# Performance work log

Measured on AMD Instinct MI355X. Metric: run time of the kernel, lower is better.

The kernel has to match this reference:

```python
import jax, jax.numpy as jnp
import numpy as np

EMBED, HID, INSIDE, OUTSIDE, EPS = 128, 64, 4, 8, 1e-5
N_NODES, N_EDGES, BATCH, SEQLEN = 16384, 262144, 64, 21


def _layernorm(x, g, b):
    m = x.mean(-1, keepdims=True)
    v = ((x - m) ** 2).mean(-1, keepdims=True)
    return (x - m) * jax.lax.rsqrt(v + EPS) * g + b


def _lstm_dir(x, Wih, Whh, bih, bhh, reverse):
    # x: [B, L, D] -> h: [B, L, HID]; PyTorch gate order i,f,g,o
    pre = jnp.einsum('bld,gd->blg', x, Wih) + bih + bhh  # [B,L,4H]
    pre = jnp.swapaxes(pre, 0, 1)  # [L,B,4H]
    h0 = jnp.zeros((x.shape[0], HID), x.dtype)

    def step(carry, xt):
        h, c = carry
        gates = xt + h @ Whh.T
        i, f, g, o = jnp.split(gates, 4, axis=-1)
        c = jax.nn.sigmoid(f) * c + jax.nn.sigmoid(i) * jnp.tanh(g)
        h = jax.nn.sigmoid(o) * jnp.tanh(c)
        return (h, c), h

    _, hs = jax.lax.scan(step, (h0, h0), pre, reverse=reverse)
    return jnp.swapaxes(hs, 0, 1)


def setup_inputs():
    key = jax.random.key(0)
    ks = jax.random.split(key, 40)
    f = jnp.float32
    N, E, B, L, D = N_NODES, N_EDGES, BATCH, SEQLEN, EMBED

    def w(k, shape, fan_in):
        return jax.random.normal(k, shape, f) * (1.0 / np.sqrt(fan_in))

    inp = {
        'x': jax.random.normal(ks[0], (N, 2561), f),
        'edge_index': jax.random.randint(ks[1], (2, E), 0, N, jnp.int32),
        'edge_attr': jax.random.normal(ks[2], (E, 3), f),
        # sorted node->graph assignment; every graph id 0..B-1 present
        'batch': ((jnp.arange(N, dtype=jnp.int32) * B) // N).astype(jnp.int32),
        'hotslice': jax.random.normal(ks[3], (B, L, 28), f),
        # randn_like noise tensors from the torch forward, made explicit inputs
        'noise_seqy': jax.random.normal(ks[4], (B, L, D), f),
        'noise_seqz': jax.random.normal(ks[5], (B, L, D), f),
        'noise_sty': jax.random.normal(ks[6], (N, D), f),
        'noise_stz': jax.random.normal(ks[7], (N, D), f),
        # AttnNN params
        'W_esm': w(ks[8], (D, 2560), 2560), 'b_esm': jnp.zeros((D,), f),
        'W_node': w(ks[9], (D, D + 1), D + 1), 'b_node': jnp.zeros((D,), f),
        'W_seq': w(ks[10], (D, 28), 28), 'b_seq': jnp.zeros((D,), f),
        # SeqStructBlock params
        'ln_seq_g': jnp.ones((D,), f), 'ln_seq_b': jnp.zeros((D,), f),
        'ln_st_g': jnp.ones((D,), f), 'ln_st_b': jnp.zeros((D,), f),
        'W_in': w(ks[11], (D, 2 * D + 3), 2 * D + 3), 'b_in': jnp.zeros((D,), f),
        'W_out': w(ks[12], (D, 2 * D + 3), 2 * D + 3), 'b_out': jnp.zeros((D,), f),
        'Wih_f': w(ks[13], (4 * HID, D), HID), 'Whh_f': w(ks[14], (4 * HID, HID), HID),
        'bih_f': jnp.zeros((4 * HID,), f), 'bhh_f': jnp.zeros((4 * HID,), f),
        'Wih_b': w(ks[15], (4 * HID, D), HID), 'Whh_b': w(ks[16], (4 * HID, HID), HID),
        'bih_b': jnp.zeros((4 * HID,), f), 'bhh_b': jnp.zeros((4 * HID,), f),
        # BatchNorm1d (eval mode: running stats)
        'bn_g': jnp.ones((D,), f), 'bn_b': jnp.zeros((D,), f),
        'bn_rm': jnp.zeros((D,), f), 'bn_rv': jnp.ones((D,), f),
    }
    return inp


def reference(x, edge_index, edge_attr, batch, hotslice,
              noise_seqy, noise_seqz, noise_sty, noise_stz,
              W_esm, b_esm, W_node, b_node, W_seq, b_seq,
              ln_seq_g, ln_seq_b, ln_st_g, ln_st_b,
              W_in, b_in, W_out, b_out,
              Wih_f, Whh_f, bih_f, bhh_f, Wih_b, Whh_b, bih_b, bhh_b,
              bn_g, bn_b, bn_rm, bn_rv):
    N = x.shape[0]
    B = hotslice.shape[0]
    src, dst = edge_index[0, 0::2], edge_index[1, 0::2]
    ea_in, ea_out = edge_attr[1::2], edge_attr[0::2]

    def ss(seq, struct):
        # bidirectional LSTM + residual + LayerNorm (dropout = identity, eval)
        hf = _lstm_dir(seq, Wih_f, Whh_f, bih_f, bhh_f, False)
        hb = _lstm_dir(seq, Wih_b, Whh_b, bih_b, bhh_b, True)
        seq = _layernorm(seq + jnp.concatenate([hf, hb], -1), ln_seq_g, ln_seq_b)
        sn = struct
        fs, fd = sn[src], sn[dst]  # [E/2, 128] gathers
        gin = jax.nn.sigmoid(jnp.concatenate([fs, fd, ea_in], -1) @ W_in.T + b_in)
        struct = struct + jax.ops.segment_sum(gin * fd, src, num_segments=N)
        gout = jax.nn.sigmoid(jnp.concatenate([fs, fd, ea_out], -1) @ W_out.T + b_out)
        struct = struct + jax.ops.segment_sum(gout * fs, dst, num_segments=N)
        return seq, _layernorm(struct, ln_st_g, ln_st_b)

    seq0 = hotslice @ W_seq.T + b_seq                       # [B,L,128]
    esm = x[:, 1:] @ W_esm.T + b_esm                        # [N,128]
    struct0 = jnp.concatenate([esm, x[:, :1]], -1) @ W_node.T + b_node  # [N,128]

    def outer(carry):
        sy, sz, ty, tz = carry

        def inner(c, _):
            szc, tzc = c
            return ss(seq0 + sy + szc, struct0 + ty + tzc), None

        (sz, tz), _ = jax.lax.scan(inner, (sz, tz), None, length=INSIDE)
        sy, ty = ss(sy + sz, ty + tz)
        return (sy, sz, ty, tz)

    carry = (noise_seqy, noise_seqz, noise_sty, noise_stz)
    carry, _ = jax.lax.scan(lambda c, _: (outer(c), None), carry, None,
                            length=OUTSIDE - 1)
    sy, sz, ty, tz = outer(carry)

    # middleSelect picks the first node of each consecutive batch run;
    # batch is sorted with every graph id present -> run starts via searchsorted
    starts = jnp.searchsorted(batch, jnp.arange(B, dtype=batch.dtype))
    feat = sy[:, 10, :] + ty[starts]                        # [B,128]
    # BatchNorm1d, eval mode (running stats)
    return (feat - bn_rm) * jax.lax.rsqrt(bn_rv + EPS) * bn_g + bn_b
```

## Files before the change

### kernel.cpp

```cpp
#include <hip/hip_runtime.h>
#include <hip/hip_fp16.h>
#include <math.h>

#define D 128
#define G4 256
#define LSEQ 21
#define EPSF 1e-5f

typedef unsigned short u16;
typedef __attribute__((ext_vector_type(8))) short bf16x8;
typedef __attribute__((ext_vector_type(4))) float f32x4;
typedef __attribute__((ext_vector_type(2))) unsigned u32x2;
typedef __attribute__((ext_vector_type(4))) unsigned u32x4;

#define MFMA16(a,b,c) __builtin_amdgcn_mfma_f32_16x16x32_bf16(a,b,c,0,0,0)

__device__ __forceinline__ float sigf(float x){ return 1.0f/(1.0f+__expf(-x)); }
__device__ __forceinline__ u16 f2bf(float x){
  unsigned u = __float_as_uint(x);
  return (u16)((u + 0x7FFFu + ((u>>16)&1u)) >> 16);
}
__device__ __forceinline__ float bf2f(u16 h){ return __uint_as_float(((unsigned)h)<<16); }
__device__ __forceinline__ unsigned pack_h2(float a, float b){
  __half2 h = __floats2half2_rn(a, b);
  return *(unsigned*)&h;
}
__device__ __forceinline__ float2 unpack_h2(unsigned u){
  __half2 h = *(__half2*)&u;
  return __half22float2(h);
}
__device__ __forceinline__ u16 f2h(float v){ __half h = __float2half(v); return *(u16*)&h; }

__device__ __forceinline__ void edge_acc(u32x4 a, uint2 g, bool valid,
                                         float2 po2, float2 w0, float2 w1, float2 w2,
                                         float& ax, float& ay){
  float e0=__uint_as_float(a.y), e1=__uint_as_float(a.z), e2=__uint_as_float(a.w);
  float2 ps0 = unpack_h2(g.x);
  float2 ps1 = unpack_h2(g.y);
  float gx = po2.x + ps0.x + e0*w0.x + e1*w1.x + e2*w2.x;
  float gy = po2.y + ps1.x + e0*w0.y + e1*w1.y + e2*w2.y;
  float mm = valid ? 1.f : 0.f;
  ax = fmaf(ps0.y*mm, sigf(gx), ax);
  ay = fmaf(ps1.y*mm, sigf(gy), ay);
}

__global__ void k_misc(int* __restrict__ starts, const int* __restrict__ batch, int N, int Bb,
                       float* __restrict__ WEin, float* __restrict__ WEout,
                       const float* __restrict__ W_in, const float* __restrict__ W_out,
                       float* __restrict__ bsum_f, float* __restrict__ bsum_b,
                       const float* __restrict__ bih_f, const float* __restrict__ bhh_f,
                       const float* __restrict__ bih_b, const float* __restrict__ bhh_b){
  int tid = threadIdx.x;
  if (tid < Bb){
    int lo = 0, hi = N;
    while (lo < hi){ int m = (lo+hi)>>1; if (batch[m] < tid) lo = m+1; else hi = m; }
    starts[tid] = lo;
  }
  for (int i = tid; i < 384; i += 256){
    int t = i >> 7, j = i & 127;
    WEin [i] = W_in [(size_t)j*259 + 256 + t];
    WEout[i] = W_out[(size_t)j*259 + 256 + t];
  }
  if (tid < 256){
    bsum_f[tid] = bih_f[tid] + bhh_f[tid];
    bsum_b[tid] = bih_b[tid] + bhh_b[tid];
  }
}

__global__ void k_packB(u16* __restrict__ PB4h, u16* __restrict__ PB4l,
                        u16* __restrict__ PBnh, u16* __restrict__ PBnl,
                        u16* __restrict__ PBEh, u16* __restrict__ PBEl,
                        const float* __restrict__ W_in, const float* __restrict__ W_out,
                        const float* __restrict__ W_node, const float* __restrict__ W_esm){
  int idx = blockIdx.x*256 + threadIdx.x;
  if (idx < 65536){
    int j = idx&7, l=(idx>>3)&63, q=idx>>9;
    int ks = q&3, nt = q>>2;
    int c = nt*16 + (l&15);
    int k = ks*32 + ((l>>4)<<3) + j;
    float v;
    if (c < 128)      v = W_in [(size_t)c*259 + k];
    else if (c < 256) v = W_in [(size_t)(c-128)*259 + 128 + k];
    else if (c < 384) v = W_out[(size_t)(c-256)*259 + k];
    else              v = W_out[(size_t)(c-384)*259 + 128 + k];
    u16 h = f2bf(v);
    PB4h[idx] = h; PB4l[idx] = f2bf(v - bf2f(h));
  } else if (idx < 65536 + 16384){
    int p = idx - 65536;
    int j = p&7, l=(p>>3)&63, q=p>>9;
    int ks = q&3, nt = q>>2;
    int c = nt*16 + (l&15);
    int k = ks*32 + ((l>>4)<<3) + j;
    float v = W_node[(size_t)c*129 + k];
    u16 h = f2bf(v);
    PBnh[p] = h; PBnl[p] = f2bf(v - bf2f(h));
  } else if (idx < 65536 + 16384 + 327680){
    int p = idx - 81920;
    int j = p&7, l=(p>>3)&63, q=p>>9;
    int ks = q%80, nt = q/80;
    int c = nt*16 + (l&15);
    int k = ks*32 + ((l>>4)<<3) + j;
    float v = W_esm[(size_t)c*2560 + k];
    u16 h = f2bf(v);
    PBEh[p] = h; PBEl[p] = f2bf(v - bf2f(h));
  }
}

__global__ void k_seq0(float* __restrict__ seq0, const float* __restrict__ hot,
                       const float* __restrict__ W_seq, const float* __restrict__ b_seq){
  int row = blockIdx.x, j = threadIdx.x;
  const float* h = hot + (size_t)row*28;
  const float* w = W_seq + (size_t)j*28;
  float acc = b_seq[j];
  #pragma unroll
  for (int k = 0; k < 28; k++) acc += h[k]*w[k];
  seq0[(size_t)row*D + j] = acc;
}

__global__ __launch_bounds__(256) void k_esm2(float* __restrict__ struct0, const float* __restrict__ x,
    const u16* __restrict__ PBEh, const u16* __restrict__ PBEl,
    const u16* __restrict__ PBnh, const u16* __restrict__ PBnl,
    const float* __restrict__ b_esm, const float* __restrict__ W_node,
    const float* __restrict__ b_node){
  __shared__ union {
    struct { u16 xh[16*72], xl[16*72]; } p1;
    struct { u16 Ah[16*136], Al[16*136]; } p2;
  } uu;
  __shared__ float esmF[16*132];
  int tid = threadIdx.x;
  int r0 = blockIdx.x*16;
  int w = tid>>6, l = tid&63;
  f32x4 acc[2];
  acc[0] = (f32x4){0.f,0.f,0.f,0.f};
  acc[1] = (f32x4){0.f,0.f,0.f,0.f};

  float xv[4];
  int rr = tid >> 5, k2i = tid & 31;
  #pragma unroll
  for (int q = 0; q < 2; q++){
    const float* src = x + (size_t)(r0+rr+8*q)*2561 + 1 + k2i*2;
    xv[2*q]   = src[0];
    xv[2*q+1] = src[1];
  }
  for (int kc = 0; kc < 2560; kc += 64){
    __syncthreads();
    unsigned* xh32 = (unsigned*)uu.p1.xh;
    unsigned* xl32 = (unsigned*)uu.p1.xl;
    #pragma unroll
    for (int q = 0; q < 2; q++){
      float v0 = xv[2*q], v1 = xv[2*q+1];
      u16 h0 = f2bf(v0), h1 = f2bf(v1);
      u16 l0 = f2bf(v0 - bf2f(h0)), l1 = f2bf(v1 - bf2f(h1));
      int r = rr + 8*q;
      xh32[r*36 + k2i] = (unsigned)h0 | ((unsigned)h1 << 16);
      xl32[r*36 + k2i] = (unsigned)l0 | ((unsigned)l1 << 16);
    }
    __syncthreads();
    if (kc + 64 < 2560){
      #pragma unroll
      for (int q = 0; q < 2; q++){
        const float* src = x + (size_t)(r0+rr+8*q)*2561 + 1 + kc + 64 + k2i*2;
        xv[2*q]   = src[0];
        xv[2*q+1] = src[1];
      }
    }
    #pragma unroll
    for (int ks = 0; ks < 2; ks++){
      bf16x8 ah, al;
      {
        int row = l&15;
        int k = ks*32 + ((l>>4)<<3);
        ah = *(const bf16x8*)&uu.p1.xh[row*72 + k];
        al = *(const bf16x8*)&uu.p1.xl[row*72 + k];
      }
      int ksg = (kc>>5) + ks;
      #pragma unroll
      for (int ctl = 0; ctl < 2; ctl++){
        int nt = w*2 + ctl;
        bf16x8 bh = *(const bf16x8*)&PBEh[((size_t)(nt*80 + ksg)*64 + l)*8];
        bf16x8 bl = *(const bf16x8*)&PBEl[((size_t)(nt*80 + ksg)*64 + l)*8];
        acc[ctl] = MFMA16(ah, bh, acc[ctl]);
        acc[ctl] = MFMA16(al, bh, acc[ctl]);
        acc[ctl] = MFMA16(ah, bl, acc[ctl]);
      }
    }
  }
  __syncthreads();
  int cq = l & 15, rqb = (l>>4)*4;
  #pragma unroll
  for (int ctl = 0; ctl < 2; ctl++){
    int coln = (w*2+ctl)*16 + cq;
    float be = b_esm[coln];
    #pragma unroll
    for (int r = 0; r < 4; r++)
      esmF[(rqb+r)*132 + coln] = acc[ctl][r] + be;
  }
  __syncthreads();
  {
    unsigned* Ah32 = (unsigned*)uu.p2.Ah;
    unsigned* Al32 = (unsigned*)uu.p2.Al;
    int rr2 = tid >> 6, k2 = tid & 63;
    #pragma unroll
    for (int q = 0; q < 4; q++){
      int r = rr2 + 4*q;
      float v0 = esmF[r*132 + k2*2];
      float v1 = esmF[r*132 + k2*2 + 1];
      u16 h0 = f2bf(v0), h1 = f2bf(v1);
      u16 l0 = f2bf(v0 - bf2f(h0)), l1 = f2bf(v1 - bf2f(h1));
      Ah32[r*68 + k2] = (unsigned)h0 | ((unsigned)h1 << 16);
      Al32[r*68 + k2] = (unsigned)l0 | ((unsigned)l1 << 16);
    }
  }
  __syncthreads();
  f32x4 acc2[2];
  acc2[0] = (f32x4){0.f,0.f,0.f,0.f};
  acc2[1] = (f32x4){0.f,0.f,0.f,0.f};
  #pragma unroll
  for (int ks = 0; ks < 4; ks++){
    bf16x8 ah, al;
    {
      int row = l&15;
      int k = ks*32 + ((l>>4)<<3);
      ah = *(const bf16x8*)&uu.p2.Ah[row*136 + k];
      al = *(const bf16x8*)&uu.p2.Al[row*136 + k];
    }
    #pragma unroll
    for (int ctl = 0; ctl < 2; ctl++){
      int nt = w*2 + ctl;
      bf16x8 bh = *(const bf16x8*)&PBnh[((size_t)(nt*4 + ks)*64 + l)*8];
      bf16x8 bl = *(const bf16x8*)&PBnl[((size_t)(nt*4 + ks)*64 + l)*8];
      acc2[ctl] = MFMA16(ah, bh, acc2[ctl]);
      acc2[ctl] = MFMA16(al, bh, acc2[ctl]);
      acc2[ctl] = MFMA16(ah, bl, acc2[ctl]);
    }
  }
  #pragma unroll
  for (int ctl = 0; ctl < 2; ctl++){
    int col = (w*2+ctl)*16 + cq;
    float wl = W_node[(size_t)col*129 + 128];
    float bn = b_node[col];
    #pragma unroll
    for (int r = 0; r < 4; r++){
      int row = r0 + rqb + r;
      float x0 = x[(size_t)row*2561];
      struct0[(size_t)row*D + col] = acc2[ctl][r] + x0*wl + bn;
    }
  }
}

__global__ void k_zero2(int* a, int* b, int n){
  int i = blockIdx.x*blockDim.x + threadIdx.x;
  if (i < n){ a[i] = 0; b[i] = 0; }
}
__global__ void k_count(int* cnt_s, int* cnt_d, const int* __restrict__ ei, int E2){
  int e = blockIdx.x*blockDim.x + threadIdx.x;
  if (e < E2){
    atomicAdd(&cnt_s[ei[2*e]], 1);
    atomicAdd(&cnt_d[ei[2*E2 + 2*e]], 1);
  }
}
__global__ __launch_bounds__(1024) void k_scanp1(const int* __restrict__ cnt_s,
                                                 const int* __restrict__ cnt_d,
                                                 int* __restrict__ part, int n, int nch){
  int arr = blockIdx.x / nch, chunk = blockIdx.x % nch;
  const int* cnt = arr ? cnt_d : cnt_s;
  int i = chunk*1024 + threadIdx.x;
  int v = (i < n) ? cnt[i] : 0;
  __shared__ int ws[16];
  #pragma unroll
  for (int o = 32; o; o >>= 1) v += __shfl_down(v, o);
  if ((threadIdx.x & 63) == 0) ws[threadIdx.x >> 6] = v;
  __syncthreads();
  if (threadIdx.x == 0){
    int t = 0;
    #pragma unroll
    for (int q = 0; q < 16; q++) t += ws[q];
    part[blockIdx.x] = t;
  }
}
__global__ void k_scanp2(int* part, int nch){
  int tid = threadIdx.x;
  if (tid < 2){
    int base = 0;
    for (int i = 0; i < nch; i++){
      int v = part[tid*nch + i];
      part[tid*nch + i] = base;
      base += v;
    }
  }
}
__global__ __launch_bounds__(1024) void k_scanp3(const int* __restrict__ cnt_s,
                                                 const int* __restrict__ cnt_d,
                                                 const int* __restrict__ part,
                                                 int* __restrict__ offs_s, int* __restrict__ offs_d,
                                                 int n, int nch){
  int arr = blockIdx.x / nch, chunk = blockIdx.x % nch;
  const int* cnt = arr ? cnt_d : cnt_s;
  int* offs = arr ? offs_d : offs_s;
  __shared__ int sh[1024];
  int tid = threadIdx.x;
  int i = chunk*1024 + tid;
  int v = (i < n) ? cnt[i] : 0;
  sh[tid] = v;
  __syncthreads();
  for (int off = 1; off < 1024; off <<= 1){
    int t = (tid >= off) ? sh[tid-off] : 0;
    __syncthreads();
    sh[tid] += t;
    __syncthreads();
  }
  int base = part[blockIdx.x];
  if (i < n) offs[i] = base + sh[tid] - v;
  if (i == n-1) offs[n] = base + sh[tid];
}
__global__ void k_copy2(int* cur_s, const int* offs_s, int* cur_d, const int* offs_d, int n){
  int i = blockIdx.x*blockDim.x + threadIdx.x;
  if (i < n){ cur_s[i] = offs_s[i]; cur_d[i] = offs_d[i]; }
}
__global__ void k_fill(const int* __restrict__ ei, const float* __restrict__ eattr, int E2,
                       int* cur_s, int4* __restrict__ adj_s,
                       int* cur_d, int4* __restrict__ adj_d){
  int e = blockIdx.x*blockDim.x + threadIdx.x;
  if (e >= E2) return;
  int s = ei[2*e];
  int d = ei[2*E2 + 2*e];
  const float* ein  = eattr + (size_t)(2*e+1)*3;
  const float* eout = eattr + (size_t)(2*e)*3;
  int ps = atomicAdd(&cur_s[s], 1);
  adj_s[ps] = make_int4(d, __float_as_int(ein[0]),  __float_as_int(ein[1]),  __float_as_int(ein[2]));
  int pd = atomicAdd(&cur_d[d], 1);
  adj_d[pd] = make_int4(s, __float_as_int(eout[0]), __float_as_int(eout[1]), __float_as_int(eout[2]));
}
__global__ void k_pad(int4* __restrict__ adj_s, int4* __restrict__ adj_d, int E2){
  int t = threadIdx.x;
  if (t < 8){
    adj_s[E2+t] = make_int4(0,0,0,0);
    adj_d[E2+t] = make_int4(0,0,0,0);
  }
}

__global__ __launch_bounds__(256) void k_seqA(
  const float* __restrict__ s0s, const float* __restrict__ sy, const float* __restrict__ sz,
  float* __restrict__ seq_in, float* __restrict__ pre_f, float* __restrict__ pre_b,
  const float* __restrict__ Wih_f, const float* __restrict__ Wih_b,
  const float* __restrict__ bsum_f, const float* __restrict__ bsum_b)
{
  __shared__ float sh[LSEQ*128];
  int tid = threadIdx.x;
  int b = blockIdx.x;
  for (int idx = tid; idx < LSEQ*128; idx += 256){
    size_t off = (size_t)b*LSEQ*128 + idx;
    float v = sy[off] + sz[off];
    if (s0s) v += s0s[off];
    sh[idx] = v;
    seq_in[off] = v;
  }
  __syncthreads();
  int g = tid;
  float accf[LSEQ], accb[LSEQ];
  float bf = bsum_f[g], bb = bsum_b[g];
  #pragma unroll
  for (int l = 0; l < LSEQ; l++){ accf[l] = bf; accb[l] = bb; }
  const float* wfp = Wih_f + (size_t)g*128;
  const float* wbp = Wih_b + (size_t)g*128;
  for (int kc = 0; kc < 128; kc += 16){
    float4 wf[4], wb[4];
    #pragma unroll
    for (int q = 0; q < 4; q++){
      wf[q] = *(const float4*)(wfp + kc + 4*q);
      wb[q] = *(const float4*)(wbp + kc + 4*q);
    }
    #pragma unroll
    for (int l = 0; l < LSEQ; l++){
      #pragma unroll
      for (int q = 0; q < 4; q++){
        float4 s4 = *(const float4*)&sh[l*128 + kc + 4*q];
        accf[l] += s4.x*wf[q].x + s4.y*wf[q].y + s4.z*wf[q].z + s4.w*wf[q].w;
        accb[l] += s4.x*wb[q].x + s4.y*wb[q].y + s4.z*wb[q].z + s4.w*wb[q].w;
      }
    }
  }
  for (int l = 0; l < LSEQ; l++){
    pre_f[((size_t)b*LSEQ + l)*G4 + g] = accf[l];
    pre_b[((size_t)b*LSEQ + l)*G4 + g] = accb[l];
  }
}

__global__ __launch_bounds__(256) void k_A(
  const float* __restrict__ s0t, const float* __restrict__ ty, const float* __restrict__ tz,
  const u16* __restrict__ PB4h, const u16* __restrict__ PB4l,
  unsigned* __restrict__ G_in, unsigned* __restrict__ G_out,
  unsigned* __restrict__ PownPk,
  const float* __restrict__ b_in, const float* __restrict__ b_out, int N)
{
  __shared__ struct { u16 Ah[32*136], Al[32*136]; float Sf[32*132]; } m;
  int tid = threadIdx.x;
  int r0 = blockIdx.x*32;
  const float4* ty4 = (const float4*)(ty + (size_t)r0*D);
  const float4* tz4 = (const float4*)(tz + (size_t)r0*D);
  const float4* s04 = s0t ? (const float4*)(s0t + (size_t)r0*D) : nullptr;
  #pragma unroll
  for (int q = 0; q < 4; q++){
    int i = tid + 256*q;
    int r = i >> 5, k4 = i & 31;
    float4 v = ty4[i];
    float4 z = tz4[i];
    v.x += z.x; v.y += z.y; v.z += z.z; v.w += z.w;
    if (s04){ float4 s = s04[i]; v.x += s.x; v.y += s.y; v.z += s.z; v.w += s.w; }
    u16 h0 = f2bf(v.x), h1 = f2bf(v.y), h2 = f2bf(v.z), h3 = f2bf(v.w);
    *(ushort4*)&m.Ah[r*136 + k4*4] = make_ushort4(h0,h1,h2,h3);
    *(ushort4*)&m.Al[r*136 + k4*4] = make_ushort4(
        f2bf(v.x - bf2f(h0)), f2bf(v.y - bf2f(h1)),
        f2bf(v.z - bf2f(h2)), f2bf(v.w - bf2f(h3)));
    *(float4*)&m.Sf[r*132 + k4*4] = v;
  }
  __syncthreads();
  int w = tid >> 6, l = tid & 63;
  f32x4 acc[2][8];
  #pragma unroll
  for (int a=0;a<2;a++)
    #pragma unroll
    for (int b=0;b<8;b++) acc[a][b] = (f32x4){0.f,0.f,0.f,0.f};
  #pragma unroll
  for (int ks = 0; ks < 4; ks++){
    bf16x8 ah[2], al[2];
    #pragma unroll
    for (int rt = 0; rt < 2; rt++){
      int row = rt*16 + (l&15);
      int k = ks*32 + ((l>>4)<<3);
      ah[rt] = *(const bf16x8*)&m.Ah[row*136 + k];
      al[rt] = *(const bf16x8*)&m.Al[row*136 + k];
    }
    #pragma unroll
    for (int ct = 0; ct < 8; ct++){
      int nt = w*8 + ct;
      bf16x8 bh = *(const bf16x8*)&PB4h[((size_t)(nt*4 + ks)*64 + l)*8];
      bf16x8 bl = *(const bf16x8*)&PB4l[((size_t)(nt*4 + ks)*64 + l)*8];
      #pragma unroll
      for (int rt = 0; rt < 2; rt++){
        acc[rt][ct] = MFMA16(ah[rt], bh, acc[rt][ct]);
        acc[rt][ct] = MFMA16(al[rt], bh, acc[rt][ct]);
        acc[rt][ct] = MFMA16(ah[rt], bl, acc[rt][ct]);
      }
    }
  }
  __syncthreads();
  unsigned* stg = (unsigned*)m.Ah;
  u16* stg16 = (u16*)m.Ah;
  int cq = l & 15, rqb = (l>>4)*4;
  if (w == 1){
    #pragma unroll
    for (int ct = 0; ct < 8; ct++){
      int coln = ct*16 + cq;
      #pragma unroll
      for (int rt = 0; rt < 2; rt++){
        #pragma unroll
        for (int r = 0; r < 4; r++){
          int lr = rt*16 + rqb + r;
          stg[lr*128 + coln] = pack_h2(acc[rt][ct][r], m.Sf[lr*132 + coln]);
        }
      }
    }
  }
  __syncthreads();
  {
    uint4* dst = (uint4*)(G_in + (size_t)r0*D);
    const uint4* src = (const uint4*)stg;
    #pragma unroll
    for (int q = 0; q < 4; q++) dst[tid + 256*q] = src[tid + 256*q];
  }
  __syncthreads();
  if (w == 2){
    #pragma unroll
    for (int ct = 0; ct < 8; ct++){
      int coln = ct*16 + cq;
      #pragma unroll
      for (int rt = 0; rt < 2; rt++){
        #pragma unroll
        for (int r = 0; r < 4; r++){
          int lr = rt*16 + rqb + r;
          stg[lr*128 + coln] = pack_h2(acc[rt][ct][r], m.Sf[lr*132 + coln]);
        }
      }
    }
  }
  __syncthreads();
  {
    uint4* dst = (uint4*)(G_out + (size_t)r0*D);
    const uint4* src = (const uint4*)stg;
    #pragma unroll
    for (int q = 0; q < 4; q++) dst[tid + 256*q] = src[tid + 256*q];
  }
  __syncthreads();
  if (w == 0 || w == 3){
    const float* bb = (w == 0) ? b_in : b_out;
    int half = (w == 0) ? 0 : 1;
    #pragma unroll
    for (int ct = 0; ct < 8; ct++){
      int coln = ct*16 + cq;
      float bc = bb[coln];
      #pragma unroll
      for (int rt = 0; rt < 2; rt++){
        #pragma unroll
        for (int r = 0; r < 4; r++){
          int lr = rt*16 + rqb + r;
          stg16[(lr*128 + coln)*2 + half] = f2h(acc[rt][ct][r] + bc);
        }
      }
    }
  }
  __syncthreads();
  {
    uint4* dst = (uint4*)(PownPk + (size_t)r0*D);
    const uint4* src = (const uint4*)stg;
    #pragma unroll
    for (int q = 0; q < 4; q++) dst[tid + 256*q] = src[tid + 256*q];
  }
}

__global__ __launch_bounds__(512) void k_B(
  const unsigned* __restrict__ G_in, const unsigned* __restrict__ G_out,
  const unsigned* __restrict__ PownPk,
  float* __restrict__ to,
  const int* __restrict__ offs_s, const int4* __restrict__ adj_s,
  const int* __restrict__ offs_d, const int4* __restrict__ adj_d,
  const float* __restrict__ WEin, const float* __restrict__ WEout,
  const float* __restrict__ ln_st_g, const float* __restrict__ ln_st_b,
  float* pre_f, float* pre_b,
  const float* __restrict__ Whh_f, const float* __restrict__ Whh_b,
  float* seq_in, float* __restrict__ so,
  const float* __restrict__ otherS, const float* __restrict__ s0s_n,
  const float* __restrict__ Wih_f, const float* __restrict__ Wih_b,
  const float* __restrict__ bsum_f, const float* __restrict__ bsum_b,
  const float* __restrict__ ln_seq_g, const float* __restrict__ ln_seq_b,
  int doNext, int N, int Bb)
{
  __shared__ union {
    struct {
      float h_hist[2][LSEQ][64];
      float hcur[2][64];
      float gsh[2][G4];
      float soL[LSEQ*128];
      float shG[LSEQ*128];
    } sq;
  } u;
  if ((int)blockIdx.x >= Bb){
    int wv = threadIdx.x >> 6, lane = threadIdx.x & 63;
    int n0 = ((blockIdx.x - Bb)*8 + wv)*4;
    const float2* WEi2 = (const float2*)WEin;
    const float2* WEo2 = (const float2*)WEout;
    float2 wi0 = WEi2[lane], wi1 = WEi2[64+lane], wi2 = WEi2[128+lane];
    float2 wo0 = WEo2[lane], wo1 = WEo2[64+lane], wo2 = WEo2[128+lane];
    float2 g2v = ((const float2*)ln_st_g)[lane], be2 = ((const float2*)ln_st_b)[lane];
    const uint2* Gi = (const uint2*)G_in;
    const uint2* Go = (const uint2*)G_out;
    #pragma unroll 1
    for (int n = n0; n < n0+4; ++n){
      u32x2 pw = *((const u32x2*)PownPk + (size_t)n*64 + lane);
      float2 pp0 = unpack_h2(pw.x), pp1 = unpack_h2(pw.y);
      float2 poI = make_float2(pp0.x, pp1.x);
      float2 poO = make_float2(pp0.y, pp1.y);
      uint2 gown = Gi[(size_t)n*64 + lane];
      float ax = 0.f, ay = 0.f;
      int j0 = __builtin_amdgcn_readfirstlane(offs_s[n]);
      int j1 = __builtin_amdgcn_readfirstlane(offs_s[n+1]);
      for (int jb = j0; jb < j1; jb += 4){
        int rem = j1 - jb;
        const u32x4* ap = (const u32x4*)adj_s + jb;
        u32x4 a0 = ap[0], a1 = ap[1], a2 = ap[2], a3 = ap[3];
        uint2 g0 = Gi[(size_t)a0.x*64 + lane];
        uint2 g1 = Gi[(size_t)a1.x*64 + lane];
        uint2 g2 = Gi[(size_t)a2.x*64 + lane];
        uint2 g3 = Gi[(size_t)a3.x*64 + lane];
        edge_acc(a0, g0, true,  poI, wi0, wi1, wi2, ax, ay);
        edge_acc(a1, g1, rem>1, poI, wi0, wi1, wi2, ax, ay);
        edge_acc(a2, g2, rem>2, poI, wi0, wi1, wi2, ax, ay);
        edge_acc(a3, g3, rem>3, poI, wi0, wi1, wi2, ax, ay);
      }
      j0 = __builtin_amdgcn_readfirstlane(offs_d[n]);
      j1 = __builtin_amdgcn_readfirstlane(offs_d[n+1]);
      for (int jb = j0; jb < j1; jb += 4){
        int rem = j1 - jb;
        const u32x4* ap = (const u32x4*)adj_d + jb;
        u32x4 a0 = ap[0], a1 = ap[1], a2 = ap[2], a3 = ap[3];
        uint2 g0 = Go[(size_t)a0.x*64 + lane];
        uint2 g1 = Go[(size_t)a1.x*64 + lane];
        uint2 g2 = Go[(size_t)a2.x*64 + lane];
        uint2 g3 = Go[(size_t)a3.x*64 + lane];
        edge_acc(a0, g0, true,  poO, wo0, wo1, wo2, ax, ay);
        edge_acc(a1, g1, rem>1, poO, wo0, wo1, wo2, ax, ay);
        edge_acc(a2, g2, rem>2, poO, wo0, wo1, wo2, ax, ay);
        edge_acc(a3, g3, rem>3, poO, wo0, wo1, wo2, ax, ay);
      }
      float vx = unpack_h2(gown.x).y + ax;
      float vy = unpack_h2(gown.y).y + ay;
      float s = vx+vy, sq = vx*vx + vy*vy;
      #pragma unroll
      for (int o = 32; o; o >>= 1){ s += __shfl_xor(s, o); sq += __shfl_xor(sq, o); }
      float mean = s*(1.f/128.f);
      float inv = rsqrtf(sq*(1.f/128.f) - mean*mean + EPSF);
      float2 o2;
      o2.x = (vx-mean)*inv*g2v.x + be2.x;
      o2.y = (vy-mean)*inv*g2v.y + be2.y;
      ((float2*)to)[(size_t)n*64 + lane] = o2;
    }
  } else {
    int b = blockIdx.x;
    int tid = threadIdx.x;
    int dir = tid >> 8, g = tid & 255;
    const float* Whh = dir ? Whh_b : Whh_f;
    const float* pre = dir ? pre_b : pre_f;
    float w[64];
    #pragma unroll
    for (int q = 0; q < 16; q++){
      float4 t4 = *(const float4*)(Whh + (size_t)g*64 + 4*q);
      w[4*q] = t4.x; w[4*q+1] = t4.y; w[4*q+2] = t4.z; w[4*q+3] = t4.w;
    }
    float c = 0.f;
    for (int t = 0; t < LSEQ; ++t){
      int tt = dir ? (LSEQ-1-t) : t;
      float gate = pre[((size_t)b*LSEQ + tt)*G4 + g];
      if (t > 0){
        #pragma unroll
        for (int q = 0; q < 16; q++){
          float4 h4 = *(const float4*)&u.sq.hcur[dir][4*q];
          gate += w[4*q]*h4.x + w[4*q+1]*h4.y + w[4*q+2]*h4.z + w[4*q+3]*h4.w;
        }
      }
      u.sq.gsh[dir][g] = gate;
      __syncthreads();
      if (g < 64){
        float iv = u.sq.gsh[dir][g], fv = u.sq.gsh[dir][64+g];
        float gv = u.sq.gsh[dir][128+g], ov = u.sq.gsh[dir][192+g];
        c = sigf(fv)*c + sigf(iv)*tanhf(gv);
        float h = sigf(ov)*tanhf(c);
        u.sq.hcur[dir][g] = h;
        u.sq.h_hist[dir][tt][g] = h;
      }
      __syncthreads();
    }
    int wv = tid >> 6, lane = tid & 63;
    for (int l = wv; l < LSEQ; l += 8){
      float2 sv = ((const float2*)(seq_in + ((size_t)b*LSEQ + l)*128))[lane];
      float hv0, hv1;
      if (lane < 32){ hv0 = u.sq.h_hist[0][l][2*lane];    hv1 = u.sq.h_hist[0][l][2*lane+1]; }
      else          { hv0 = u.sq.h_hist[1][l][2*lane-64]; hv1 = u.sq.h_hist[1][l][2*lane-63]; }
      float vx = sv.x + hv0, vy = sv.y + hv1;
      float s = vx+vy, sq = vx*vx + vy*vy;
      #pragma unroll
      for (int o = 32; o; o >>= 1){ s += __shfl_xor(s, o); sq += __shfl_xor(sq, o); }
      float mean = s*(1.f/128.f);
      float inv = rsqrtf(sq*(1.f/128.f) - mean*mean + EPSF);
      float2 g2 = ((const float2*)ln_seq_g)[lane], b2 = ((const float2*)ln_seq_b)[lane];
      float2 o2;
      o2.x = (vx-mean)*inv*g2.x + b2.x;
      o2.y = (vy-mean)*inv*g2.y + b2.y;
      ((float2*)(so + ((size_t)b*LSEQ + l)*128))[lane] = o2;
      u.sq.soL[l*128 + 2*lane]     = o2.x;
      u.sq.soL[l*128 + 2*lane + 1] = o2.y;
    }
    if (!doNext) return;
    __syncthreads();
    {
      const float4* oS4 = (const float4*)(otherS + (size_t)b*LSEQ*128);
      const float4* s04 = s0s_n ? (const float4*)(s0s_n + (size_t)b*LSEQ*128) : nullptr;
      float4* gi4 = (float4*)(seq_in + (size_t)b*LSEQ*128);
      for (int idx = tid; idx < LSEQ*32; idx += 512){
        float4 v = *(const float4*)&u.sq.soL[idx*4];
        float4 o = oS4[idx];
        v.x += o.x; v.y += o.y; v.z += o.z; v.w += o.w;
        if (s04){ float4 s0 = s04[idx]; v.x += s0.x; v.y += s0.y; v.z += s0.z; v.w += s0.w; }
        *(float4*)&u.sq.shG[idx*4] = v;
        gi4[idx] = v;
      }
    }
    __syncthreads();
    {
      int g2 = tid & 255;
      int dn = tid >> 8;
      const float* wp = (dn ? Wih_b : Wih_f) + (size_t)g2*128;
      float bsv = dn ? bsum_b[g2] : bsum_f[g2];
      float accv[LSEQ];
      #pragma unroll
      for (int l = 0; l < LSEQ; l++) accv[l] = bsv;
      for (int kc = 0; kc < 128; kc += 16){
        float4 wf[4];
        #pragma unroll
        for (int q = 0; q < 4; q++) wf[q] = *(const float4*)(wp + kc + 4*q);
        #pragma unroll
        for (int l = 0; l < LSEQ; l++){
          #pragma unroll
          for (int q = 0; q < 4; q++){
            float4 s4 = *(const float4*)&u.sq.shG[l*128 + kc + 4*q];
            accv[l] += s4.x*wf[q].x + s4.y*wf[q].y + s4.z*wf[q].z + s4.w*wf[q].w;
          }
        }
      }
      float* dst = dn ? pre_b : pre_f;
      for (int l = 0; l < LSEQ; l++)
        dst[((size_t)b*LSEQ + l)*G4 + g2] = accv[l];
    }
  }
}

__global__ void k_final(float* __restrict__ out, const float* __restrict__ sy,
                        const float* __restrict__ ty, const int* __restrict__ starts,
                        const float* __restrict__ g, const float* __restrict__ b,
                        const float* __restrict__ rm, const float* __restrict__ rv, int Bb){
  int i = blockIdx.x*blockDim.x + threadIdx.x;
  if (i >= Bb*D) return;
  int bb = i >> 7, d = i & 127;
  float feat = sy[((size_t)bb*LSEQ + 10)*D + d] + ty[(size_t)starts[bb]*D + d];
  out[i] = (feat - rm[d])*rsqrtf(rv[d]+EPSF)*g[d] + b[d];
}

extern "C" void kernel_launch(void* const* d_in, const int* in_sizes, int n_in,
                              void* d_out, int out_size, void* d_ws, size_t ws_size,
                              hipStream_t stream)
{
  const float* x        = (const float*)d_in[0];
  const int*   ei       = (const int*)  d_in[1];
  const float* eattr    = (const float*)d_in[2];
  const int*   batch    = (const int*)  d_in[3];
  const float* hotslice = (const float*)d_in[4];
  const float* nsy      = (const float*)d_in[5];
  const float* nsz      = (const float*)d_in[6];
  const float* nty      = (const float*)d_in[7];
  const float* ntz      = (const float*)d_in[8];
  const float* W_esm    = (const float*)d_in[9];
  const float* b_esm    = (const float*)d_in[10];
  const float* W_node   = (const float*)d_in[11];
  const float* b_node   = (const float*)d_in[12];
  const float* W_seq    = (const float*)d_in[13];
  const float* b_seq    = (const float*)d_in[14];
  const float* ln_seq_g = (const float*)d_in[15];
  const float* ln_seq_b = (const float*)d_in[16];
  const float* ln_st_g  = (const float*)d_in[17];
  const float* ln_st_b  = (const float*)d_in[18];
  const float* W_in     = (const float*)d_in[19];
  const float* b_in     = (const float*)d_in[20];
  const float* W_out    = (const float*)d_in[21];
  const float* b_out    = (const float*)d_in[22];
  const float* Wih_f    = (const float*)d_in[23];
  const float* Whh_f    = (const float*)d_in[24];
  const float* bih_f    = (const float*)d_in[25];
  const float* bhh_f    = (const float*)d_in[26];
  const float* Wih_b    = (const float*)d_in[27];
  const float* Whh_b    = (const float*)d_in[28];
  const float* bih_b    = (const float*)d_in[29];
  const float* bhh_b    = (const float*)d_in[30];
  const float* bn_g     = (const float*)d_in[31];
  const float* bn_b     = (const float*)d_in[32];
  const float* bn_rm    = (const float*)d_in[33];
  const float* bn_rv    = (const float*)d_in[34];

  const int N  = in_sizes[0] / 2561;
  const int E  = in_sizes[1] / 2;
  const int E2 = E / 2;
  const int Bb = in_sizes[4] / (LSEQ*28);
  const int BL = Bb*LSEQ;

  char* p = (char*)d_ws;
  auto alloc = [&](size_t bytes)->void*{
    void* r = (void*)p; p += (bytes + 255) & ~(size_t)255; return r;
  };
  float*    seq0      = (float*)alloc((size_t)BL*D*4);
  float*    sy        = (float*)alloc((size_t)BL*D*4);
  float*    sz        = (float*)alloc((size_t)BL*D*4);
  float*    seq_in    = (float*)alloc((size_t)BL*D*4);
  float*    pre_f     = (float*)alloc((size_t)BL*G4*4);
  float*    pre_b     = (float*)alloc((size_t)BL*G4*4);
  float*    struct0   = (float*)alloc((size_t)N*D*4);
  float*    ty        = (float*)alloc((size_t)N*D*4);
  float*    tz        = (float*)alloc((size_t)N*D*4);
  unsigned* G_in      = (unsigned*)alloc((size_t)N*D*4);
  unsigned* G_out     = (unsigned*)alloc((size_t)N*D*4);
  unsigned* PownPk    = (unsigned*)alloc((size_t)N*D*4);
  u16*      PB4h      = (u16*)alloc(65536*2);
  u16*      PB4l      = (u16*)alloc(65536*2);
  u16*      PBnh      = (u16*)alloc(16384*2);
  u16*      PBnl      = (u16*)alloc(16384*2);
  u16*      PBEh      = (u16*)alloc(327680*2);
  u16*      PBEl      = (u16*)alloc(327680*2);
  float*    WEin      = (float*)alloc(384*4);
  float*    WEout     = (float*)alloc(384*4);
  float*    bsum_f    = (float*)alloc(256*4);
  float*    bsum_b    = (float*)alloc(256*4);
  int*      starts    = (int*)alloc((size_t)Bb*4);
  int*      cnt_s     = (int*)alloc((size_t)N*4);
  int*      cnt_d     = (int*)alloc((size_t)N*4);
  int*      offs_s    = (int*)alloc((size_t)(N+1)*4);
  int*      offs_d    = (int*)alloc((size_t)(N+1)*4);
  int*      cur_s     = (int*)alloc((size_t)N*4);
  int*      cur_d     = (int*)alloc((size_t)N*4);
  int*      part      = (int*)alloc(2*((size_t)(N+1023)>>10)*4 + 256);
  int4*     adj_s     = (int4*)alloc((size_t)(E2+8)*16);
  int4*     adj_d     = (int4*)alloc((size_t)(E2+8)*16);
  (void)ws_size; (void)n_in; (void)out_size;

  hipMemcpyAsync(sy, nsy, (size_t)BL*D*4, hipMemcpyDeviceToDevice, stream);
  hipMemcpyAsync(sz, nsz, (size_t)BL*D*4, hipMemcpyDeviceToDevice, stream);
  hipMemcpyAsync(ty, nty, (size_t)N*D*4, hipMemcpyDeviceToDevice, stream);
  hipMemcpyAsync(tz, ntz, (size_t)N*D*4, hipMemcpyDeviceToDevice, stream);

  k_misc<<<1, 256, 0, stream>>>(starts, batch, N, Bb, WEin, WEout, W_in, W_out,
                                bsum_f, bsum_b, bih_f, bhh_f, bih_b, bhh_b);
  k_packB<<<1600, 256, 0, stream>>>(PB4h, PB4l, PBnh, PBnl, PBEh, PBEl,
                                    W_in, W_out, W_node, W_esm);
  k_seq0<<<BL, 128, 0, stream>>>(seq0, hotslice, W_seq, b_seq);
  k_esm2<<<N/16, 256, 0, stream>>>(struct0, x, PBEh, PBEl, PBnh, PBnl,
                                   b_esm, W_node, b_node);
  k_zero2<<<(N+255)/256, 256, 0, stream>>>(cnt_s, cnt_d, N);
  k_count<<<(E2+255)/256, 256, 0, stream>>>(cnt_s, cnt_d, ei, E2);
  {
    int nch = (N + 1023) >> 10;
    k_scanp1<<<2*nch, 1024, 0, stream>>>(cnt_s, cnt_d, part, N, nch);
    k_scanp2<<<1, 64, 0, stream>>>(part, nch);
    k_scanp3<<<2*nch, 1024, 0, stream>>>(cnt_s, cnt_d, part, offs_s, offs_d, N, nch);
  }
  k_copy2<<<(N+255)/256, 256, 0, stream>>>(cur_s, offs_s, cur_d, offs_d, N);
  k_fill<<<(E2+255)/256, 256, 0, stream>>>(ei, eattr, E2, cur_s, adj_s, cur_d, adj_d);
  k_pad<<<1, 64, 0, stream>>>(adj_s, adj_d, E2);
  k_seqA<<<Bb, 256, 0, stream>>>(seq0, sy, sz, seq_in, pre_f, pre_b,
                                 Wih_f, Wih_b, bsum_f, bsum_b);

  const int NB = N/32;

  for (int o = 0; o < 8; ++o){
    for (int it = 0; it < 5; ++it){
      int gi = o*5 + it;
      bool inner = (it < 4);
      const float* s0t = inner ? struct0 : nullptr;
      float* to_ = inner ? tz : ty;
      float* so_ = inner ? sz : sy;
      const float* otherS = inner ? sy : sz;
      int itn = (gi+1) % 5;
      const float* s0s_n = (itn < 4) ? seq0 : nullptr;
      int doNext = (gi < 39) ? 1 : 0;
      k_A<<<NB, 256, 0, stream>>>(s0t, ty, tz, PB4h, PB4l,
                                  G_in, G_out, PownPk, b_in, b_out, N);
      k_B<<<Bb + NB, 512, 0, stream>>>(G_in, G_out, PownPk, to_,
                                       offs_s, adj_s, offs_d, adj_d,
                                       WEin, WEout, ln_st_g, ln_st_b,
                                       pre_f, pre_b, Whh_f, Whh_b,
                                       seq_in, so_, otherS, s0s_n,
                                       Wih_f, Wih_b, bsum_f, bsum_b,
                                       ln_seq_g, ln_seq_b, doNext, N, Bb);
    }
  }

  k_final<<<(Bb*D+255)/256, 256, 0, stream>>>((float*)d_out, sy, ty, starts,
                                              bn_g, bn_b, bn_rm, bn_rv, Bb);
}
```

Measured before the change: 3.573 ms.

## Retile ESM projection to 32 rows per 512-thread block; prefetch next node data

The ESM/node projection kernel now processes 32 rows per block with 8 waves. Each wave owns one 16-column tile and reuses its B fragments across two row tiles, where before each wave owned two column tiles and loaded two B fragment sets per k-step. This halves the global B-weight loads per row and the block count, at the cost of larger shared memory and more registers per thread. Separately, the graph-structure branch prefetches the next node's own packed projections and gate values one iteration ahead to hide load latency.

```diff
diff --git a/kernel.cpp b/kernel.cpp
--- a/kernel.cpp
+++ b/kernel.cpp
@@ -117,18 +117,18 @@
   seq0[(size_t)row*D + j] = acc;
 }
 
-__global__ __launch_bounds__(256) void k_esm2(float* __restrict__ struct0, const float* __restrict__ x,
+__global__ __launch_bounds__(512) void k_esm2(float* __restrict__ struct0, const float* __restrict__ x,
     const u16* __restrict__ PBEh, const u16* __restrict__ PBEl,
     const u16* __restrict__ PBnh, const u16* __restrict__ PBnl,
     const float* __restrict__ b_esm, const float* __restrict__ W_node,
     const float* __restrict__ b_node){
   __shared__ union {
-    struct { u16 xh[16*72], xl[16*72]; } p1;
-    struct { u16 Ah[16*136], Al[16*136]; } p2;
+    struct { u16 xh[32*72], xl[32*72]; } p1;
+    struct { u16 Ah[32*136], Al[32*136]; } p2;
   } uu;
-  __shared__ float esmF[16*132];
+  __shared__ float esmF[32*132];
   int tid = threadIdx.x;
-  int r0 = blockIdx.x*16;
+  int r0 = blockIdx.x*32;
   int w = tid>>6, l = tid&63;
   f32x4 acc[2];
   acc[0] = (f32x4){0.f,0.f,0.f,0.f};
@@ -138,7 +138,7 @@
   int rr = tid >> 5, k2i = tid & 31;
   #pragma unroll
   for (int q = 0; q < 2; q++){
-    const float* src = x + (size_t)(r0+rr+8*q)*2561 + 1 + k2i*2;
+    const float* src = x + (size_t)(r0+rr+16*q)*2561 + 1 + k2i*2;
     xv[2*q]   = src[0];
     xv[2*q+1] = src[1];
   }
@@ -151,7 +151,7 @@
       float v0 = xv[2*q], v1 = xv[2*q+1];
       u16 h0 = f2bf(v0), h1 = f2bf(v1);
       u16 l0 = f2bf(v0 - bf2f(h0)), l1 = f2bf(v1 - bf2f(h1));
-      int r = rr + 8*q;
+      int r = rr + 16*q;
       xh32[r*36 + k2i] = (unsigned)h0 | ((unsigned)h1 << 16);
       xl32[r*36 + k2i] = (unsigned)l0 | ((unsigned)l1 << 16);
     }
@@ -159,41 +159,42 @@
     if (kc + 64 < 2560){
       #pragma unroll
       for (int q = 0; q < 2; q++){
-        const float* src = x + (size_t)(r0+rr+8*q)*2561 + 1 + kc + 64 + k2i*2;
+        const float* src = x + (size_t)(r0+rr+16*q)*2561 + 1 + kc + 64 + k2i*2;
         xv[2*q]   = src[0];
         xv[2*q+1] = src[1];
       }
     }
     #pragma unroll
     for (int ks = 0; ks < 2; ks++){
-      bf16x8 ah, al;
-      {
-        int row = l&15;
+      bf16x8 ah[2], al[2];
+      #pragma unroll
+      for (int rt = 0; rt < 2; rt++){
+        int row = rt*16 + (l&15);
         int k = ks*32 + ((l>>4)<<3);
-        ah = *(const bf16x8*)&uu.p1.xh[row*72 + k];
-        al = *(const bf16x8*)&uu.p1.xl[row*72 + k];
+        ah[rt] = *(const bf16x8*)&uu.p1.xh[row*72 + k];
+        al[rt] = *(const bf16x8*)&uu.p1.xl[row*72 + k];
       }
       int ksg = (kc>>5) + ks;
-      #pragma unroll
-      for (int ctl = 0; ctl < 2; ctl++){
-        int nt = w*2 + ctl;
-        bf16x8 bh = *(const bf16x8*)&PBEh[((size_t)(nt*80 + ksg)*64 + l)*8];
-        bf16x8 bl = *(const bf16x8*)&PBEl[((size_t)(nt*80 + ksg)*64 + l)*8];
-        acc[ctl] = MFMA16(ah, bh, acc[ctl]);
-        acc[ctl] = MFMA16(al, bh, acc[ctl]);
-        acc[ctl] = MFMA16(ah, bl, acc[ctl]);
+      bf16x8 bh = *(const bf16x8*)&PBEh[((size_t)(w*80 + ksg)*64 + l)*8];
+      bf16x8 bl = *(const bf16x8*)&PBEl[((size_t)(w*80 + ksg)*64 + l)*8];
+      #pragma unroll
+      for (int rt = 0; rt < 2; rt++){
+        acc[rt] = MFMA16(ah[rt], bh, acc[rt]);
+        acc[rt] = MFMA16(al[rt], bh, acc[rt]);
+        acc[rt] = MFMA16(ah[rt], bl, acc[rt]);
       }
     }
   }
   __syncthreads();
   int cq = l & 15, rqb = (l>>4)*4;
-  #pragma unroll
-  for (int ctl = 0; ctl < 2; ctl++){
-    int coln = (w*2+ctl)*16 + cq;
+  {
+    int coln = w*16 + cq;
     float be = b_esm[coln];
     #pragma unroll
-    for (int r = 0; r < 4; r++)
-      esmF[(rqb+r)*132 + coln] = acc[ctl][r] + be;
+    for (int rt = 0; rt < 2; rt++)
+      #pragma unroll
+      for (int r = 0; r < 4; r++)
+        esmF[(rt*16+rqb+r)*132 + coln] = acc[rt][r] + be;
   }
   __syncthreads();
   {
@@ -202,7 +203,7 @@
     int rr2 = tid >> 6, k2 = tid & 63;
     #pragma unroll
     for (int q = 0; q < 4; q++){
-      int r = rr2 + 4*q;
+      int r = rr2 + 8*q;
       float v0 = esmF[r*132 + k2*2];
       float v1 = esmF[r*132 + k2*2 + 1];
       u16 h0 = f2bf(v0), h1 = f2bf(v1);
@@ -217,34 +218,35 @@
   acc2[1] = (f32x4){0.f,0.f,0.f,0.f};
   #pragma unroll
   for (int ks = 0; ks < 4; ks++){
-    bf16x8 ah, al;
-    {
-      int row = l&15;
+    bf16x8 ah[2], al[2];
+    #pragma unroll
+    for (int rt = 0; rt < 2; rt++){
+      int row = rt*16 + (l&15);
       int k = ks*32 + ((l>>4)<<3);
-      ah = *(const bf16x8*)&uu.p2.Ah[row*136 + k];
-      al = *(const bf16x8*)&uu.p2.Al[row*136 + k];
-    }
-    #pragma unroll
-    for (int ctl = 0; ctl < 2; ctl++){
-      int nt = w*2 + ctl;
-      bf16x8 bh = *(const bf16x8*)&PBnh[((size_t)(nt*4 + ks)*64 + l)*8];
-      bf16x8 bl = *(const bf16x8*)&PBnl[((size_t)(nt*4 + ks)*64 + l)*8];
-      acc2[ctl] = MFMA16(ah, bh, acc2[ctl]);
-      acc2[ctl] = MFMA16(al, bh, acc2[ctl]);
-      acc2[ctl] = MFMA16(ah, bl, acc2[ctl]);
-    }
-  }
-  #pragma unroll
-  for (int ctl = 0; ctl < 2; ctl++){
-    int col = (w*2+ctl)*16 + cq;
+      ah[rt] = *(const bf16x8*)&uu.p2.Ah[row*136 + k];
+      al[rt] = *(const bf16x8*)&uu.p2.Al[row*136 + k];
+    }
+    bf16x8 bh = *(const bf16x8*)&PBnh[((size_t)(w*4 + ks)*64 + l)*8];
+    bf16x8 bl = *(const bf16x8*)&PBnl[((size_t)(w*4 + ks)*64 + l)*8];
+    #pragma unroll
+    for (int rt = 0; rt < 2; rt++){
+      acc2[rt] = MFMA16(ah[rt], bh, acc2[rt]);
+      acc2[rt] = MFMA16(al[rt], bh, acc2[rt]);
+      acc2[rt] = MFMA16(ah[rt], bl, acc2[rt]);
+    }
+  }
+  {
+    int col = w*16 + cq;
     float wl = W_node[(size_t)col*129 + 128];
     float bn = b_node[col];
     #pragma unroll
-    for (int r = 0; r < 4; r++){
-      int row = r0 + rqb + r;
-      float x0 = x[(size_t)row*2561];
-      struct0[(size_t)row*D + col] = acc2[ctl][r] + x0*wl + bn;
-    }
+    for (int rt = 0; rt < 2; rt++)
+      #pragma unroll
+      for (int r = 0; r < 4; r++){
+        int row = r0 + rt*16 + rqb + r;
+        float x0 = x[(size_t)row*2561];
+        struct0[(size_t)row*D + col] = acc2[rt][r] + x0*wl + bn;
+      }
   }
 }
 
@@ -554,13 +556,19 @@
     float2 g2v = ((const float2*)ln_st_g)[lane], be2 = ((const float2*)ln_st_b)[lane];
     const uint2* Gi = (const uint2*)G_in;
     const uint2* Go = (const uint2*)G_out;
+    u32x2 pwN = *((const u32x2*)PownPk + (size_t)n0*64 + lane);
+    uint2 gownN = Gi[(size_t)n0*64 + lane];
     #pragma unroll 1
     for (int n = n0; n < n0+4; ++n){
-      u32x2 pw = *((const u32x2*)PownPk + (size_t)n*64 + lane);
+      u32x2 pw = pwN;
+      uint2 gown = gownN;
+      if (n+1 < n0+4){
+        pwN = *((const u32x2*)PownPk + (size_t)(n+1)*64 + lane);
+        gownN = Gi[(size_t)(n+1)*64 + lane];
+      }
       float2 pp0 = unpack_h2(pw.x), pp1 = unpack_h2(pw.y);
       float2 poI = make_float2(pp0.x, pp1.x);
       float2 poO = make_float2(pp0.y, pp1.y);
-      uint2 gown = Gi[(size_t)n*64 + lane];
       float ax = 0.f, ay = 0.f;
       int j0 = __builtin_amdgcn_readfirstlane(offs_s[n]);
       int j1 = __builtin_amdgcn_readfirstlane(offs_s[n+1]);
@@ -808,7 +816,7 @@
   k_packB<<<1600, 256, 0, stream>>>(PB4h, PB4l, PBnh, PBnl, PBEh, PBEl,
                                     W_in, W_out, W_node, W_esm);
   k_seq0<<<BL, 128, 0, stream>>>(seq0, hotslice, W_seq, b_seq);
-  k_esm2<<<N/16, 256, 0, stream>>>(struct0, x, PBEh, PBEl, PBnh, PBnl,
+  k_esm2<<<N/32, 512, 0, stream>>>(struct0, x, PBEh, PBEl, PBnh, PBnl,
                                    b_esm, W_node, b_node);
   k_zero2<<<(N+255)/256, 256, 0, stream>>>(cnt_s, cnt_d, N);
   k_count<<<(E2+255)/256, 256, 0, stream>>>(cnt_s, cnt_d, ei, E2);
```

Result: no change. 3.554 ms (-0.6%).
